# Performance work log

Hardware: AMD Instinct MI355X
Metric: run time of the kernel (lower is better)

## Reference

```python
import jax, jax.numpy as jnp
import numpy as np


def log_g(x):
    # log of g(x) where g(x) = x + 0.5 for x >= 0 else sigmoid(x)
    return jnp.where(x >= 0, jnp.log(jnp.where(x >= 0, x, 0.0) + 0.5), -jax.nn.softplus(-x))


def mingru_layer(x, h0, W, b):
    # x: (B,S,Din), h0: (B,1,H) positive, W: (2H,Din), b: (2H,)
    gh = jnp.einsum('bsd,ed->bse', x, W) + b
    gate, hidden = jnp.split(gh, 2, axis=-1)
    log_z = -jax.nn.softplus(-gate)        # log sigmoid(gate)
    log_coeffs = -jax.nn.softplus(gate)    # log (1 - sigmoid(gate))
    log_values = jnp.concatenate([jnp.log(h0), log_z + log_g(hidden)], axis=1)  # (B,S+1,H)
    a_star = jnp.pad(jnp.cumsum(log_coeffs, axis=1), ((0, 0), (1, 0), (0, 0)))  # (B,S+1,H)
    log_h = a_star + jax.lax.cumlogsumexp(log_values - a_star, axis=1)
    return jnp.exp(log_h)[:, 1:]  # (B,S,H)


def setup_inputs() -> dict:
    key = jax.random.key(0)
    ks = jax.random.split(key, 6)
    B, S, D, H = 8, 2048, 1024, 1024
    L = 2
    s = 0.02
    return {
        'x': jax.random.normal(ks[0], (B, S, D), jnp.float32),
        'h': jax.random.uniform(ks[1], (L, B, 1, H), jnp.float32, 0.05, 1.0),
        'w0': jax.random.normal(ks[2], (2 * H, D), jnp.float32) * s,
        'b0': jax.random.normal(ks[3], (2 * H,), jnp.float32) * s,
        'w1': jax.random.normal(ks[4], (2 * H, H), jnp.float32) * s,
        'b1': jax.random.normal(ks[5], (2 * H,), jnp.float32) * s,
    }


def reference(x, h, w0, b0, w1, b1):
    # layer 0 (residual, align = Identity since input_dims == hidden_dims)
    out0 = mingru_layer(x, h[0], w0, b0)
    h0_final = out0[:, -1:]
    inp = out0 + x
    # layer 1 (last layer: residual, no dropout after)
    out1 = mingru_layer(inp, h[1], w1, b1)
    h1_final = out1[:, -1:]
    out = out1 + inp
    h_final = jnp.stack([h0_final, h1_final])  # (L,B,1,H)
    return out, h_final
```

## Files before the change

### kernel.cpp

```cpp
#include <hip/hip_runtime.h>
#include <hip/hip_bf16.h>
#include <cstdint>
#include <cstddef>

#define GAS __attribute__((address_space(1)))
#define LAS __attribute__((address_space(3)))

typedef __attribute__((ext_vector_type(8))) __bf16 bf16x8;
typedef __attribute__((ext_vector_type(4))) float f32x4;

constexpr int kB = 8, kS = 2048, kK = 1024, kH = 1024;
constexpr int kM = kB * kS;
constexpr int kN2 = 2 * kH;
constexpr int BM = 256, BK = 32;
constexpr int NKT = kK / BK;

constexpr size_t kOffXb   = 0;
constexpr size_t kOffW0   = 33554432;
constexpr size_t kOffW1   = 37748736;
constexpr size_t kOffA    = 41943040;
constexpr size_t kOffG    = 75497472;
constexpr size_t kOffCA   = 109051904;
constexpr size_t kOffCV   = 111149056;
constexpr size_t kOffHst  = 113246208;
constexpr size_t kWsNeed  = 115343360;

__device__ __forceinline__ ushort f2bf(float f) {
    union { float f; uint32_t u; } v; v.f = f;
    uint32_t r = v.u + 0x7FFFu + ((v.u >> 16) & 1u);
    return (ushort)(r >> 16);
}
__device__ __forceinline__ float bf2f(ushort u) {
    union { uint32_t u; float f; } v; v.u = (uint32_t)u << 16;
    return v.f;
}

constexpr int QX = kM * kK / 4;
constexpr int QW = kN2 * kK / 4;
__global__ void cvt3_kernel(const float* __restrict__ x, const float* __restrict__ w0,
                            const float* __restrict__ w1,
                            ushort* __restrict__ xb, ushort* __restrict__ w0b,
                            ushort* __restrict__ w1b)
{
    int i = blockIdx.x * 256 + threadIdx.x;
    const float* s; ushort* d;
    if (i < QX)            { s = x  + (size_t)i * 4;            d = xb  + (size_t)i * 4; }
    else if (i < QX + QW)  { int k = i - QX;      s = w0 + (size_t)k * 4; d = w0b + (size_t)k * 4; }
    else                   { int k = i - QX - QW; s = w1 + (size_t)k * 4; d = w1b + (size_t)k * 4; }
    f32x4 v = *reinterpret_cast<const f32x4*>(s);
    ushort4 o;
    o.x = f2bf(v.x); o.y = f2bf(v.y); o.z = f2bf(v.z); o.w = f2bf(v.w);
    *reinterpret_cast<ushort4*>(d) = o;
}

__global__ __launch_bounds__(512, 1)
void gemm_scan_kernel(const ushort* __restrict__ A, const ushort* __restrict__ W,
                      const float* __restrict__ bias,
                      ushort* __restrict__ Apref, ushort* __restrict__ Vpref,
                      float* __restrict__ cA, float* __restrict__ cV)
{
    __shared__ ushort smem[69632];

    const int tid  = threadIdx.x;
    const int lane = tid & 63;
    const int wv   = tid >> 6;
    const int wm   = wv >> 2;
    const int wn   = wv & 3;

    const int bid = blockIdx.x;
    const int sid = (bid & 7) * 64 + (bid >> 3);
    const int tm  = sid >> 3;
    const int tn  = sid & 7;
    const int m0  = tm * BM;
    const int j0  = tn * 128;

    f32x4 acc[8][4];
#pragma unroll
    for (int i = 0; i < 8; ++i)
#pragma unroll
        for (int j = 0; j < 4; ++j) acc[i][j] = (f32x4){0.f, 0.f, 0.f, 0.f};

    const int srow  = wv * 16 + (lane >> 2);
    const int sslot = (lane & 3) ^ ((lane >> 3) & 3);
    const int scol  = sslot * 8;

    const ushort* ga0 = A + (size_t)(m0 + srow) * kK + scol;
    const ushort* ga1 = ga0 + (size_t)128 * kK;
    const ushort* gb0 = W + (size_t)(j0 + srow) * kK + scol;
    const ushort* gb1 = W + (size_t)(1024 + j0 + srow) * kK + scol;

    char* lds = (char*)smem;
    const int ldsw = wv * 1024;

    const int rslot = (lane >> 4) ^ ((lane >> 1) & 3);
    const int rb    = (lane & 15) * 64 + rslot * 16;
    const int aoff  = wm * 8192 + rb;
    const int boff  = 16384 + wn * 4096 + rb;

#define VMWAIT(N) asm volatile("s_waitcnt vmcnt(" #N ")" ::: "memory")

#define STAGE_A(SBUF) do {                                                       \
    __builtin_amdgcn_global_load_lds((const GAS void*)(ga0),                     \
        (LAS void*)(lds + (SBUF) * 32768 + ldsw),          16, 0, 0);            \
    __builtin_amdgcn_global_load_lds((const GAS void*)(ga1),                     \
        (LAS void*)(lds + (SBUF) * 32768 + 8192  + ldsw),  16, 0, 0);            \
  } while (0)

#define STAGE_B(SBUF) do {                                                       \
    __builtin_amdgcn_global_load_lds((const GAS void*)(gb0),                     \
        (LAS void*)(lds + (SBUF) * 32768 + 16384 + ldsw),  16, 0, 0);            \
    __builtin_amdgcn_global_load_lds((const GAS void*)(gb1),                     \
        (LAS void*)(lds + (SBUF) * 32768 + 24576 + ldsw),  16, 0, 0);            \
    ga0 += BK; ga1 += BK; gb0 += BK; gb1 += BK;                                  \
  } while (0)

#define TILE_GEN(BUF, SA, SB, EW) do {                                           \
    bf16x8 bf_[4], af_[4];                                                       \
    _Pragma("unroll")                                                            \
    for (int nf_ = 0; nf_ < 4; ++nf_)                                            \
        bf_[nf_] = *reinterpret_cast<const bf16x8*>(                             \
            lds + (BUF) * 32768 + boff + nf_ * 1024);                            \
    _Pragma("unroll")                                                            \
    for (int mf_ = 0; mf_ < 4; ++mf_)                                            \
        af_[mf_] = *reinterpret_cast<const bf16x8*>(                             \
            lds + (BUF) * 32768 + aoff + mf_ * 1024);                            \
    SA;                                                                          \
    __builtin_amdgcn_s_barrier();                                                \
    asm volatile("s_waitcnt lgkmcnt(0)" ::: "memory");                           \
    __builtin_amdgcn_sched_barrier(0);                                           \
    __builtin_amdgcn_s_setprio(1);                                               \
    _Pragma("unroll")                                                            \
    for (int mf_ = 0; mf_ < 4; ++mf_)                                            \
        _Pragma("unroll")                                                        \
        for (int nf_ = 0; nf_ < 4; ++nf_)                                        \
            acc[mf_][nf_] = __builtin_amdgcn_mfma_f32_16x16x32_bf16(             \
                af_[mf_], bf_[nf_], acc[mf_][nf_], 0, 0, 0);                     \
    __builtin_amdgcn_s_setprio(0);                                               \
    __builtin_amdgcn_s_barrier();                                                \
    _Pragma("unroll")                                                            \
    for (int mf_ = 0; mf_ < 4; ++mf_)                                            \
        af_[mf_] = *reinterpret_cast<const bf16x8*>(                             \
            lds + (BUF) * 32768 + aoff + 4096 + mf_ * 1024);                     \
    SB;                                                                          \
    __builtin_amdgcn_s_barrier();                                                \
    asm volatile("s_waitcnt lgkmcnt(0)" ::: "memory");                           \
    __builtin_amdgcn_sched_barrier(0);                                           \
    __builtin_amdgcn_s_setprio(1);                                               \
    _Pragma("unroll")                                                            \
    for (int mf_ = 0; mf_ < 4; ++mf_)                                            \
        _Pragma("unroll")                                                        \
        for (int nf_ = 0; nf_ < 4; ++nf_)                                        \
            acc[4 + mf_][nf_] = __builtin_amdgcn_mfma_f32_16x16x32_bf16(         \
                af_[mf_], bf_[nf_], acc[4 + mf_][nf_], 0, 0, 0);                 \
    __builtin_amdgcn_s_setprio(0);                                               \
    EW;                                                                          \
    __builtin_amdgcn_s_barrier();                                                \
  } while (0)

#define TILE(BUF, SBUF) TILE_GEN(BUF, STAGE_A(SBUF), STAGE_B(SBUF), VMWAIT(4))
#define TAIL0(BUF)      TILE_GEN(BUF, (void)0, (void)0, VMWAIT(0))
#define TAIL1(BUF)      TILE_GEN(BUF, (void)0, (void)0, (void)0)

    STAGE_A(0); STAGE_B(0);
    STAGE_A(1); STAGE_B(1);
    VMWAIT(4);
    __builtin_amdgcn_s_barrier();

    for (int g = 0; g < 7; ++g) {
        TILE(0, 2);
        TILE(1, 3);
        TILE(2, 0);
        TILE(3, 1);
    }
    TILE(0, 2);
    TILE(1, 3);
    TAIL0(2);
    TAIL1(3);

#undef TILE
#undef TAIL0
#undef TAIL1
#undef TILE_GEN
#undef STAGE_A
#undef STAGE_B
#undef VMWAIT

    ushort* a_lds = smem;
    ushort* g_lds = smem + 33792;
    float*  sumA  = (float*)(smem + 67584);
    float*  sumV  = sumA + 512;

    {
        const bool isG = (wn < 2);
        ushort* tgt = isG ? a_lds : g_lds;
        const int jl = (wn & 1) * 64;
        float bn[4];
#pragma unroll
        for (int nf = 0; nf < 4; ++nf)
            bn[nf] = bias[(isG ? 0 : 1024) + j0 + jl + nf * 16 + (lane & 15)];
#pragma unroll
        for (int mf = 0; mf < 8; ++mf) {
#pragma unroll
            for (int i = 0; i < 4; ++i) {
                const int m = wm * 128 + mf * 16 + (lane >> 4) * 4 + i;
#pragma unroll
                for (int nf = 0; nf < 4; ++nf) {
                    float val = acc[mf][nf][i] + bn[nf];
                    float r;
                    if (isG) r = 1.f / (1.f + __expf(val));
                    else     r = (val >= 0.f) ? val + 0.5f : 1.f / (1.f + __expf(-val));
                    tgt[m * 132 + jl + nf * 16 + (lane & 15)] = f2bf(r);
                }
            }
        }
    }
    __syncthreads();

    {
        const int j  = tid & 127;
        const int sg = tid >> 7;
        float A1 = 1.f, V1 = 0.f;
#pragma unroll 4
        for (int t = 0; t < 64; ++t) {
            const int s = sg * 64 + t;
            float a = bf2f(a_lds[s * 132 + j]);
            float g = bf2f(g_lds[s * 132 + j]);
            V1 = a * V1 + (1.f - a) * g;
            A1 *= a;
        }
        sumA[sg * 128 + j] = A1;
        sumV[sg * 128 + j] = V1;
        __syncthreads();
        float Ar = 1.f, Vr = 0.f;
        for (int k = 0; k < sg; ++k) {
            float Ak = sumA[k * 128 + j], Vk = sumV[k * 128 + j];
            Vr = Ak * Vr + Vk;
            Ar *= Ak;
        }
        ushort* ApG = Apref + (size_t)(m0 + sg * 64) * kH + j0 + j;
        ushort* VpG = Vpref + (size_t)(m0 + sg * 64) * kH + j0 + j;
#pragma unroll 4
        for (int t = 0; t < 64; ++t) {
            const int s = sg * 64 + t;
            float a = bf2f(a_lds[s * 132 + j]);
            float g = bf2f(g_lds[s * 132 + j]);
            Vr = a * Vr + (1.f - a) * g;
            Ar *= a;
            *ApG = f2bf(Ar);
            *VpG = f2bf(Vr);
            ApG += kH; VpG += kH;
        }
        if (sg == 3) {
            const int b = tm >> 3, c = tm & 7;
            cA[((b * 8 + c) << 10) + j0 + j] = Ar;
            cV[((b * 8 + c) << 10) + j0 + j] = Vr;
        }
    }
}

__global__ void scan_chunks_kernel(const float* __restrict__ cA, const float* __restrict__ cV,
                                   const float* __restrict__ h0, float* __restrict__ hstart,
                                   float* __restrict__ hfin)
{
    int idx = blockIdx.x * 256 + threadIdx.x;
    int j = idx & 1023, b = idx >> 10;
    float h = h0[(b << 10) + j];
    for (int c = 0; c < 8; ++c) {
        int o = ((b * 8 + c) << 10) + j;
        hstart[o] = h;
        h = cA[o] * h + cV[o];
    }
    hfin[(b << 10) + j] = h;
}

template<bool WRITE_F32>
__global__ void apply_kernel(const ushort* __restrict__ Ap, const ushort* __restrict__ Vp,
                             const float* __restrict__ hst, const ushort* __restrict__ res,
                             void* __restrict__ outp)
{
    size_t i = ((size_t)blockIdx.x * 256 + threadIdx.x) * 4;
    int m = (int)(i >> 10);
    int j = (int)(i & 1023);
    int b = m >> 11, s = m & 2047, c = s >> 8;
    f32x4 hcs = *reinterpret_cast<const f32x4*>(hst + (((b * 8 + c) << 10) + j));
    ushort4 Au = *reinterpret_cast<const ushort4*>(Ap + i);
    ushort4 Vu = *reinterpret_cast<const ushort4*>(Vp + i);
    ushort4 Ru = *reinterpret_cast<const ushort4*>(res + i);
    f32x4 o;
    o.x = bf2f(Au.x) * hcs.x + bf2f(Vu.x) + bf2f(Ru.x);
    o.y = bf2f(Au.y) * hcs.y + bf2f(Vu.y) + bf2f(Ru.y);
    o.z = bf2f(Au.z) * hcs.z + bf2f(Vu.z) + bf2f(Ru.z);
    o.w = bf2f(Au.w) * hcs.w + bf2f(Vu.w) + bf2f(Ru.w);
    if (WRITE_F32) {
        *reinterpret_cast<f32x4*>((float*)outp + i) = o;
    } else {
        ushort4 ob;
        ob.x = f2bf(o.x); ob.y = f2bf(o.y); ob.z = f2bf(o.z); ob.w = f2bf(o.w);
        *reinterpret_cast<ushort4*>((ushort*)outp + i) = ob;
    }
}

extern "C" void kernel_launch(void* const* d_in, const int* in_sizes, int n_in,
                              void* d_out, int out_size, void* d_ws, size_t ws_size,
                              hipStream_t stream)
{
    const float* x  = (const float*)d_in[0];
    const float* h  = (const float*)d_in[1];
    const float* w0 = (const float*)d_in[2];
    const float* b0 = (const float*)d_in[3];
    const float* w1 = (const float*)d_in[4];
    const float* b1 = (const float*)d_in[5];
    float* out = (float*)d_out;
    char* ws = (char*)d_ws;

    if (ws_size < kWsNeed) return;

    ushort* xb   = (ushort*)(ws + kOffXb);
    ushort* inpb = (ushort*)(ws + kOffXb);
    ushort* w0b  = (ushort*)(ws + kOffW0);
    ushort* w1b  = (ushort*)(ws + kOffW1);
    ushort* Ap   = (ushort*)(ws + kOffA);
    ushort* Vp   = (ushort*)(ws + kOffG);
    float*  cA   = (float*)(ws + kOffCA);
    float*  cV   = (float*)(ws + kOffCV);
    float*  hst  = (float*)(ws + kOffHst);

    float* out_h = out + (size_t)kM * kH;

    cvt3_kernel<<<(QX + 2 * QW) / 256, 256, 0, stream>>>(x, w0, w1, xb, w0b, w1b);

    const int gemm_grid  = (kM / BM) * (kN2 / 256);
    const int apply_grid = kM * kH / 4 / 256;

    gemm_scan_kernel<<<gemm_grid, 512, 0, stream>>>(xb, w0b, b0, Ap, Vp, cA, cV);
    scan_chunks_kernel<<<32, 256, 0, stream>>>(cA, cV, h, hst, out_h);
    apply_kernel<false><<<apply_grid, 256, 0, stream>>>(Ap, Vp, hst, xb, inpb);

    gemm_scan_kernel<<<gemm_grid, 512, 0, stream>>>(inpb, w1b, b1, Ap, Vp, cA, cV);
    scan_chunks_kernel<<<32, 256, 0, stream>>>(cA, cV, h + (size_t)kB * kH, hst, out_h + (size_t)kB * kH);
    apply_kernel<true><<<apply_grid, 256, 0, stream>>>(Ap, Vp, hst, inpb, out);
}
```

Measured before the change: 270.9 us.

## Restructure GEMM main loop to BK=64 with two-stage double buffering

The K-step doubles from 32 to 64. The four-stage 32KB LDS ring becomes a two-stage 64KB ring, and each tile is split into four phases that each issue part of the next tile's global-to-LDS loads. Loop iterations and loop overhead are halved. The prefetch distance is shorter, and the vmcnt waits now sit mid-tile, so global-load latency may be less well hidden.

```diff
diff --git a/kernel.cpp b/kernel.cpp
--- a/kernel.cpp
+++ b/kernel.cpp
@@ -12,7 +12,7 @@
 constexpr int kB = 8, kS = 2048, kK = 1024, kH = 1024;
 constexpr int kM = kB * kS;
 constexpr int kN2 = 2 * kH;
-constexpr int BM = 256, BK = 32;
+constexpr int BM = 256, BK = 64;
 constexpr int NKT = kK / BK;
 
 constexpr size_t kOffXb   = 0;
@@ -95,94 +95,116 @@
     const int rslot = (lane >> 4) ^ ((lane >> 1) & 3);
     const int rb    = (lane & 15) * 64 + rslot * 16;
     const int aoff  = wm * 8192 + rb;
-    const int boff  = 16384 + wn * 4096 + rb;
+    const int boff  = 32768 + wn * 4096 + rb;
 
 #define VMWAIT(N) asm volatile("s_waitcnt vmcnt(" #N ")" ::: "memory")
 
-#define STAGE_A(SBUF) do {                                                       \
-    __builtin_amdgcn_global_load_lds((const GAS void*)(ga0),                     \
-        (LAS void*)(lds + (SBUF) * 32768 + ldsw),          16, 0, 0);            \
-    __builtin_amdgcn_global_load_lds((const GAS void*)(ga1),                     \
-        (LAS void*)(lds + (SBUF) * 32768 + 8192  + ldsw),  16, 0, 0);            \
+#define STG_A(SBUF, KH) do {                                                     \
+    __builtin_amdgcn_global_load_lds((const GAS void*)(ga0 + (KH) * 32),         \
+        (LAS void*)(lds + (SBUF) * 65536 + (KH) * 16384 + ldsw),        16, 0, 0); \
+    __builtin_amdgcn_global_load_lds((const GAS void*)(ga1 + (KH) * 32),         \
+        (LAS void*)(lds + (SBUF) * 65536 + (KH) * 16384 + 8192 + ldsw), 16, 0, 0); \
   } while (0)
 
-#define STAGE_B(SBUF) do {                                                       \
-    __builtin_amdgcn_global_load_lds((const GAS void*)(gb0),                     \
-        (LAS void*)(lds + (SBUF) * 32768 + 16384 + ldsw),  16, 0, 0);            \
-    __builtin_amdgcn_global_load_lds((const GAS void*)(gb1),                     \
-        (LAS void*)(lds + (SBUF) * 32768 + 24576 + ldsw),  16, 0, 0);            \
-    ga0 += BK; ga1 += BK; gb0 += BK; gb1 += BK;                                  \
+#define STG_B(SBUF, KH) do {                                                     \
+    __builtin_amdgcn_global_load_lds((const GAS void*)(gb0 + (KH) * 32),         \
+        (LAS void*)(lds + (SBUF) * 65536 + 32768 + (KH) * 16384 + ldsw), 16, 0, 0); \
+    __builtin_amdgcn_global_load_lds((const GAS void*)(gb1 + (KH) * 32),         \
+        (LAS void*)(lds + (SBUF) * 65536 + 32768 + (KH) * 16384 + 8192 + ldsw), 16, 0, 0); \
   } while (0)
 
-#define TILE_GEN(BUF, SA, SB, EW) do {                                           \
+#define PH_SYNC                                                                  \
+    __builtin_amdgcn_s_barrier();                                                \
+    asm volatile("s_waitcnt lgkmcnt(0)" ::: "memory");                           \
+    __builtin_amdgcn_sched_barrier(0)
+
+#define MFMA16(BASE)                                                             \
+    __builtin_amdgcn_s_setprio(1);                                               \
+    _Pragma("unroll")                                                            \
+    for (int mf_ = 0; mf_ < 4; ++mf_)                                            \
+        _Pragma("unroll")                                                        \
+        for (int nf_ = 0; nf_ < 4; ++nf_)                                        \
+            acc[(BASE) + mf_][nf_] = __builtin_amdgcn_mfma_f32_16x16x32_bf16(    \
+                af_[mf_], bf_[nf_], acc[(BASE) + mf_][nf_], 0, 0, 0);            \
+    __builtin_amdgcn_s_setprio(0)
+
+#define TILE64(BUF, S0, S1, S2, S3, EW1, EW3) do {                               \
     bf16x8 bf_[4], af_[4];                                                       \
+                          \
     _Pragma("unroll")                                                            \
     for (int nf_ = 0; nf_ < 4; ++nf_)                                            \
         bf_[nf_] = *reinterpret_cast<const bf16x8*>(                             \
-            lds + (BUF) * 32768 + boff + nf_ * 1024);                            \
+            lds + (BUF) * 65536 + boff + nf_ * 1024);                            \
     _Pragma("unroll")                                                            \
     for (int mf_ = 0; mf_ < 4; ++mf_)                                            \
         af_[mf_] = *reinterpret_cast<const bf16x8*>(                             \
-            lds + (BUF) * 32768 + aoff + mf_ * 1024);                            \
-    SA;                                                                          \
-    __builtin_amdgcn_s_barrier();                                                \
-    asm volatile("s_waitcnt lgkmcnt(0)" ::: "memory");                           \
-    __builtin_amdgcn_sched_barrier(0);                                           \
-    __builtin_amdgcn_s_setprio(1);                                               \
-    _Pragma("unroll")                                                            \
-    for (int mf_ = 0; mf_ < 4; ++mf_)                                            \
-        _Pragma("unroll")                                                        \
-        for (int nf_ = 0; nf_ < 4; ++nf_)                                        \
-            acc[mf_][nf_] = __builtin_amdgcn_mfma_f32_16x16x32_bf16(             \
-                af_[mf_], bf_[nf_], acc[mf_][nf_], 0, 0, 0);                     \
-    __builtin_amdgcn_s_setprio(0);                                               \
-    __builtin_amdgcn_s_barrier();                                                \
+            lds + (BUF) * 65536 + aoff + mf_ * 1024);                            \
+    S0;                                                                          \
+    PH_SYNC;                                                                     \
+    MFMA16(0);                                                                   \
+    __builtin_amdgcn_s_barrier();                                                \
+                                                \
     _Pragma("unroll")                                                            \
     for (int mf_ = 0; mf_ < 4; ++mf_)                                            \
         af_[mf_] = *reinterpret_cast<const bf16x8*>(                             \
-            lds + (BUF) * 32768 + aoff + 4096 + mf_ * 1024);                     \
-    SB;                                                                          \
-    __builtin_amdgcn_s_barrier();                                                \
-    asm volatile("s_waitcnt lgkmcnt(0)" ::: "memory");                           \
-    __builtin_amdgcn_sched_barrier(0);                                           \
-    __builtin_amdgcn_s_setprio(1);                                               \
-    _Pragma("unroll")                                                            \
-    for (int mf_ = 0; mf_ < 4; ++mf_)                                            \
-        _Pragma("unroll")                                                        \
-        for (int nf_ = 0; nf_ < 4; ++nf_)                                        \
-            acc[4 + mf_][nf_] = __builtin_amdgcn_mfma_f32_16x16x32_bf16(         \
-                af_[mf_], bf_[nf_], acc[4 + mf_][nf_], 0, 0, 0);                 \
-    __builtin_amdgcn_s_setprio(0);                                               \
-    EW;                                                                          \
+            lds + (BUF) * 65536 + aoff + 4096 + mf_ * 1024);                     \
+    S1;                                                                          \
+    PH_SYNC;                                                                     \
+    MFMA16(4);                                                                   \
+    EW1;                                                                         \
+    __builtin_amdgcn_s_barrier();                                                \
+                                                             \
+    _Pragma("unroll")                                                            \
+    for (int nf_ = 0; nf_ < 4; ++nf_)                                            \
+        bf_[nf_] = *reinterpret_cast<const bf16x8*>(                             \
+            lds + (BUF) * 65536 + 16384 + boff + nf_ * 1024);                    \
+    _Pragma("unroll")                                                            \
+    for (int mf_ = 0; mf_ < 4; ++mf_)                                            \
+        af_[mf_] = *reinterpret_cast<const bf16x8*>(                             \
+            lds + (BUF) * 65536 + 16384 + aoff + mf_ * 1024);                    \
+    S2;                                                                          \
+    PH_SYNC;                                                                     \
+    MFMA16(0);                                                                   \
+    __builtin_amdgcn_s_barrier();                                                \
+                                                             \
+    _Pragma("unroll")                                                            \
+    for (int mf_ = 0; mf_ < 4; ++mf_)                                            \
+        af_[mf_] = *reinterpret_cast<const bf16x8*>(                             \
+            lds + (BUF) * 65536 + 16384 + aoff + 4096 + mf_ * 1024);             \
+    S3;                                                                          \
+    PH_SYNC;                                                                     \
+    MFMA16(4);                                                                   \
+    EW3;                                                                         \
     __builtin_amdgcn_s_barrier();                                                \
   } while (0)
 
-#define TILE(BUF, SBUF) TILE_GEN(BUF, STAGE_A(SBUF), STAGE_B(SBUF), VMWAIT(4))
-#define TAIL0(BUF)      TILE_GEN(BUF, (void)0, (void)0, VMWAIT(0))
-#define TAIL1(BUF)      TILE_GEN(BUF, (void)0, (void)0, (void)0)
-
-    STAGE_A(0); STAGE_B(0);
-    STAGE_A(1); STAGE_B(1);
+#define ADV do { ga0 += BK; ga1 += BK; gb0 += BK; gb1 += BK; } while (0)
+#define TILE(BUF) TILE64(BUF,                                                    \
+    STG_A((BUF) ^ 1, 0), STG_B((BUF) ^ 1, 0),                                    \
+    STG_A((BUF) ^ 1, 1), do { STG_B((BUF) ^ 1, 1); ADV; } while (0),             \
+    VMWAIT(4), VMWAIT(4))
+#define TAIL(BUF) TILE64(BUF, (void)0, (void)0, (void)0, (void)0, VMWAIT(0), (void)0)
+
+    STG_A(0, 0); STG_B(0, 0); STG_A(0, 1); STG_B(0, 1);
+    ADV;
     VMWAIT(4);
     __builtin_amdgcn_s_barrier();
 
     for (int g = 0; g < 7; ++g) {
-        TILE(0, 2);
-        TILE(1, 3);
-        TILE(2, 0);
-        TILE(3, 1);
-    }
-    TILE(0, 2);
-    TILE(1, 3);
-    TAIL0(2);
-    TAIL1(3);
+        TILE(0);
+        TILE(1);
+    }
+    TILE(0);
+    TAIL(1);
 
 #undef TILE
-#undef TAIL0
-#undef TAIL1
-#undef TILE_GEN
-#undef STAGE_A
-#undef STAGE_B
+#undef TAIL
+#undef TILE64
+#undef MFMA16
+#undef PH_SYNC
+#undef STG_A
+#undef STG_B
+#undef ADV
 #undef VMWAIT
 
     ushort* a_lds = smem;
```

Result: no change. 270.3 us (-0.2%).

## Halve GEMM row tile to 128 with 2 blocks per CU and vectorized chunk scan

Applied to the files above, without the earlier changes.

Reworks the fused GEMM+scan kernel to use 128-row tiles with 256 threads and two resident blocks per CU. The LDS pipeline changes from four stages to three, and the sequence is split into 16 chunks instead of 8. The in-block scan now processes four hidden columns per thread with vector LDS loads and global stores. The aim is better occupancy and latency hiding, plus fewer serial scan steps per thread. The cost is that each block loads W for fewer rows, so more global traffic per FLOP, and the cross-chunk scan gets longer.

```diff
diff --git a/kernel.cpp b/kernel.cpp
--- a/kernel.cpp
+++ b/kernel.cpp
@@ -12,8 +12,9 @@
 constexpr int kB = 8, kS = 2048, kK = 1024, kH = 1024;
 constexpr int kM = kB * kS;
 constexpr int kN2 = 2 * kH;
-constexpr int BM = 256, BK = 32;
+constexpr int BM = 128, BK = 32;
 constexpr int NKT = kK / BK;
+constexpr int kChunks = 16;
 
 constexpr size_t kOffXb   = 0;
 constexpr size_t kOffW0   = 33554432;
@@ -21,8 +22,8 @@
 constexpr size_t kOffA    = 41943040;
 constexpr size_t kOffG    = 75497472;
 constexpr size_t kOffCA   = 109051904;
-constexpr size_t kOffCV   = 111149056;
-constexpr size_t kOffHst  = 113246208;
+constexpr size_t kOffCV   = 109576192;
+constexpr size_t kOffHst  = 110100480;
 constexpr size_t kWsNeed  = 115343360;
 
 __device__ __forceinline__ ushort f2bf(float f) {
@@ -53,77 +54,82 @@
     *reinterpret_cast<ushort4*>(d) = o;
 }
 
-__global__ __launch_bounds__(512, 1)
+__global__ __launch_bounds__(256, 2)
 void gemm_scan_kernel(const ushort* __restrict__ A, const ushort* __restrict__ W,
                       const float* __restrict__ bias,
                       ushort* __restrict__ Apref, ushort* __restrict__ Vpref,
                       float* __restrict__ cA, float* __restrict__ cV)
 {
-    __shared__ ushort smem[69632];
+    __shared__ ushort smem[37888];
 
     const int tid  = threadIdx.x;
     const int lane = tid & 63;
     const int wv   = tid >> 6;
-    const int wm   = wv >> 2;
-    const int wn   = wv & 3;
+    const int wm   = wv >> 1;
+    const int wn   = wv & 1;
 
     const int bid = blockIdx.x;
-    const int sid = (bid & 7) * 64 + (bid >> 3);
+    const int sid = (bid & 7) * 128 + (bid >> 3);
     const int tm  = sid >> 3;
     const int tn  = sid & 7;
     const int m0  = tm * BM;
     const int j0  = tn * 128;
-
-    f32x4 acc[8][4];
-#pragma unroll
-    for (int i = 0; i < 8; ++i)
-#pragma unroll
-        for (int j = 0; j < 4; ++j) acc[i][j] = (f32x4){0.f, 0.f, 0.f, 0.f};
-
-    const int srow  = wv * 16 + (lane >> 2);
-    const int sslot = (lane & 3) ^ ((lane >> 3) & 3);
+    const int b   = tm >> 4;
+    const int c   = tm & 15;
+
+    f32x4 acc[4][8];
+#pragma unroll
+    for (int i = 0; i < 4; ++i)
+#pragma unroll
+        for (int j = 0; j < 8; ++j) acc[i][j] = (f32x4){0.f, 0.f, 0.f, 0.f};
+
+    const int srow  = tid >> 2;
+    const int sslot = (tid & 3) ^ ((tid >> 3) & 3);
     const int scol  = sslot * 8;
+    const int tid16 = tid * 16;
 
     const ushort* ga0 = A + (size_t)(m0 + srow) * kK + scol;
-    const ushort* ga1 = ga0 + (size_t)128 * kK;
     const ushort* gb0 = W + (size_t)(j0 + srow) * kK + scol;
     const ushort* gb1 = W + (size_t)(1024 + j0 + srow) * kK + scol;
 
     char* lds = (char*)smem;
-    const int ldsw = wv * 1024;
 
     const int rslot = (lane >> 4) ^ ((lane >> 1) & 3);
     const int rb    = (lane & 15) * 64 + rslot * 16;
-    const int aoff  = wm * 8192 + rb;
-    const int boff  = 16384 + wn * 4096 + rb;
+    const int aoff  = wm * 4096 + rb;
+    const int boff  = 8192 + wn * 8192 + rb;
 
 #define VMWAIT(N) asm volatile("s_waitcnt vmcnt(" #N ")" ::: "memory")
 
-#define STAGE_A(SBUF) do {                                                       \
+#define STG3A(S) do {                                                            \
     __builtin_amdgcn_global_load_lds((const GAS void*)(ga0),                     \
-        (LAS void*)(lds + (SBUF) * 32768 + ldsw),          16, 0, 0);            \
-    __builtin_amdgcn_global_load_lds((const GAS void*)(ga1),                     \
-        (LAS void*)(lds + (SBUF) * 32768 + 8192  + ldsw),  16, 0, 0);            \
+        (LAS void*)(lds + (S) * 24576 + tid16),          16, 0, 0);              \
+    __builtin_amdgcn_global_load_lds((const GAS void*)(ga0 + 65536),             \
+        (LAS void*)(lds + (S) * 24576 + 4096 + tid16),   16, 0, 0);              \
+    __builtin_amdgcn_global_load_lds((const GAS void*)(gb0),                     \
+        (LAS void*)(lds + (S) * 24576 + 8192 + tid16),   16, 0, 0);              \
   } while (0)
 
-#define STAGE_B(SBUF) do {                                                       \
-    __builtin_amdgcn_global_load_lds((const GAS void*)(gb0),                     \
-        (LAS void*)(lds + (SBUF) * 32768 + 16384 + ldsw),  16, 0, 0);            \
+#define STG3B(S) do {                                                            \
+    __builtin_amdgcn_global_load_lds((const GAS void*)(gb0 + 65536),             \
+        (LAS void*)(lds + (S) * 24576 + 12288 + tid16),  16, 0, 0);              \
     __builtin_amdgcn_global_load_lds((const GAS void*)(gb1),                     \
-        (LAS void*)(lds + (SBUF) * 32768 + 24576 + ldsw),  16, 0, 0);            \
-    ga0 += BK; ga1 += BK; gb0 += BK; gb1 += BK;                                  \
+        (LAS void*)(lds + (S) * 24576 + 16384 + tid16),  16, 0, 0);              \
+    __builtin_amdgcn_global_load_lds((const GAS void*)(gb1 + 65536),             \
+        (LAS void*)(lds + (S) * 24576 + 20480 + tid16),  16, 0, 0);              \
+    ga0 += BK; gb0 += BK; gb1 += BK;                                             \
   } while (0)
 
 #define TILE_GEN(BUF, SA, SB, EW) do {                                           \
-    bf16x8 bf_[4], af_[4];                                                       \
+    bf16x8 af_[4], bf_[4];                                                       \
+    _Pragma("unroll")                                                            \
+    for (int mf_ = 0; mf_ < 4; ++mf_)                                            \
+        af_[mf_] = *reinterpret_cast<const bf16x8*>(                             \
+            lds + (BUF) * 24576 + aoff + mf_ * 1024);                            \
     _Pragma("unroll")                                                            \
     for (int nf_ = 0; nf_ < 4; ++nf_)                                            \
         bf_[nf_] = *reinterpret_cast<const bf16x8*>(                             \
-            lds + (BUF) * 32768 + boff + nf_ * 1024);                            \
-    _Pragma("unroll")                                                            \
-    for (int mf_ = 0; mf_ < 4; ++mf_)                                            \
-        af_[mf_] = *reinterpret_cast<const bf16x8*>(                             \
-            lds + (BUF) * 32768 + aoff + mf_ * 1024);                            \
+            lds + (BUF) * 24576 + boff + nf_ * 1024);                            \
     SA;                                                                          \
     __builtin_amdgcn_s_barrier();                                                \
     asm volatile("s_waitcnt lgkmcnt(0)" ::: "memory");                           \
@@ -138,9 +144,9 @@
     __builtin_amdgcn_s_setprio(0);                                               \
     __builtin_amdgcn_s_barrier();                                                \
     _Pragma("unroll")                                                            \
-    for (int mf_ = 0; mf_ < 4; ++mf_)                                            \
-        af_[mf_] = *reinterpret_cast<const bf16x8*>(                             \
-            lds + (BUF) * 32768 + aoff + 4096 + mf_ * 1024);                     \
+    for (int nf_ = 0; nf_ < 4; ++nf_)                                            \
+        bf_[nf_] = *reinterpret_cast<const bf16x8*>(                             \
+            lds + (BUF) * 24576 + boff + (4 + nf_) * 1024);                      \
     SB;                                                                          \
     __builtin_amdgcn_s_barrier();                                                \
     asm volatile("s_waitcnt lgkmcnt(0)" ::: "memory");                           \
@@ -150,66 +156,62 @@
     for (int mf_ = 0; mf_ < 4; ++mf_)                                            \
         _Pragma("unroll")                                                        \
         for (int nf_ = 0; nf_ < 4; ++nf_)                                        \
-            acc[4 + mf_][nf_] = __builtin_amdgcn_mfma_f32_16x16x32_bf16(         \
-                af_[mf_], bf_[nf_], acc[4 + mf_][nf_], 0, 0, 0);                 \
+            acc[mf_][4 + nf_] = __builtin_amdgcn_mfma_f32_16x16x32_bf16(         \
+                af_[mf_], bf_[nf_], acc[mf_][4 + nf_], 0, 0, 0);                 \
     __builtin_amdgcn_s_setprio(0);                                               \
     EW;                                                                          \
     __builtin_amdgcn_s_barrier();                                                \
   } while (0)
 
-#define TILE(BUF, SBUF) TILE_GEN(BUF, STAGE_A(SBUF), STAGE_B(SBUF), VMWAIT(4))
+#define TILE(BUF, SBUF) TILE_GEN(BUF, STG3A(SBUF), STG3B(SBUF), VMWAIT(6))
 #define TAIL0(BUF)      TILE_GEN(BUF, (void)0, (void)0, VMWAIT(0))
 #define TAIL1(BUF)      TILE_GEN(BUF, (void)0, (void)0, (void)0)
 
-    STAGE_A(0); STAGE_B(0);
-    STAGE_A(1); STAGE_B(1);
-    VMWAIT(4);
+    STG3A(0); STG3B(0);
+    STG3A(1); STG3B(1);
+    VMWAIT(6);
     __builtin_amdgcn_s_barrier();
 
-    for (int g = 0; g < 7; ++g) {
+    for (int g = 0; g < 10; ++g) {
         TILE(0, 2);
-        TILE(1, 3);
-        TILE(2, 0);
-        TILE(3, 1);
-    }
-    TILE(0, 2);
-    TILE(1, 3);
-    TAIL0(2);
-    TAIL1(3);
+        TILE(1, 0);
+        TILE(2, 1);
+    }
+    TAIL0(0);
+    TAIL1(1);
 
 #undef TILE
 #undef TAIL0
 #undef TAIL1
 #undef TILE_GEN
-#undef STAGE_A
-#undef STAGE_B
+#undef STG3A
+#undef STG3B
 #undef VMWAIT
 
     ushort* a_lds = smem;
-    ushort* g_lds = smem + 33792;
-    float*  sumA  = (float*)(smem + 67584);
-    float*  sumV  = sumA + 512;
+    ushort* g_lds = smem + 16896;
+    f32x4*  sA4   = (f32x4*)(lds + 67584);
+    f32x4*  sV4   = (f32x4*)(lds + 71680);
 
     {
-        const bool isG = (wn < 2);
+        const bool isG = (wn == 0);
         ushort* tgt = isG ? a_lds : g_lds;
-        const int jl = (wn & 1) * 64;
-        float bn[4];
-#pragma unroll
-        for (int nf = 0; nf < 4; ++nf)
-            bn[nf] = bias[(isG ? 0 : 1024) + j0 + jl + nf * 16 + (lane & 15)];
-#pragma unroll
-        for (int mf = 0; mf < 8; ++mf) {
+        float bn[8];
+#pragma unroll
+        for (int nf = 0; nf < 8; ++nf)
+            bn[nf] = bias[(isG ? 0 : 1024) + j0 + nf * 16 + (lane & 15)];
+#pragma unroll
+        for (int mf = 0; mf < 4; ++mf) {
 #pragma unroll
             for (int i = 0; i < 4; ++i) {
-                const int m = wm * 128 + mf * 16 + (lane >> 4) * 4 + i;
-#pragma unroll
-                for (int nf = 0; nf < 4; ++nf) {
+                const int m = wm * 64 + mf * 16 + (lane >> 4) * 4 + i;
+#pragma unroll
+                for (int nf = 0; nf < 8; ++nf) {
                     float val = acc[mf][nf][i] + bn[nf];
                     float r;
                     if (isG) r = 1.f / (1.f + __expf(val));
                     else     r = (val >= 0.f) ? val + 0.5f : 1.f / (1.f + __expf(-val));
-                    tgt[m * 132 + jl + nf * 16 + (lane & 15)] = f2bf(r);
+                    tgt[m * 132 + nf * 16 + (lane & 15)] = f2bf(r);
                 }
             }
         }
@@ -217,43 +219,52 @@
     __syncthreads();
 
     {
-        const int j  = tid & 127;
-        const int sg = tid >> 7;
-        float A1 = 1.f, V1 = 0.f;
+        const int jq = tid & 31;
+        const int sg = tid >> 5;
+        f32x4 A1 = (f32x4){1.f, 1.f, 1.f, 1.f};
+        f32x4 V1 = (f32x4){0.f, 0.f, 0.f, 0.f};
 #pragma unroll 4
-        for (int t = 0; t < 64; ++t) {
-            const int s = sg * 64 + t;
-            float a = bf2f(a_lds[s * 132 + j]);
-            float g = bf2f(g_lds[s * 132 + j]);
+        for (int t = 0; t < 16; ++t) {
+            const int s = sg * 16 + t;
+            ushort4 au = *reinterpret_cast<const ushort4*>(a_lds + s * 132 + jq * 4);
+            ushort4 gu = *reinterpret_cast<const ushort4*>(g_lds + s * 132 + jq * 4);
+            f32x4 a = (f32x4){bf2f(au.x), bf2f(au.y), bf2f(au.z), bf2f(au.w)};
+            f32x4 g = (f32x4){bf2f(gu.x), bf2f(gu.y), bf2f(gu.z), bf2f(gu.w)};
             V1 = a * V1 + (1.f - a) * g;
             A1 *= a;
         }
-        sumA[sg * 128 + j] = A1;
-        sumV[sg * 128 + j] = V1;
+        sA4[sg * 32 + jq] = A1;
+        sV4[sg * 32 + jq] = V1;
         __syncthreads();
-        float Ar = 1.f, Vr = 0.f;
+        f32x4 Ar = (f32x4){1.f, 1.f, 1.f, 1.f};
+        f32x4 Vr = (f32x4){0.f, 0.f, 0.f, 0.f};
         for (int k = 0; k < sg; ++k) {
-            float Ak = sumA[k * 128 + j], Vk = sumV[k * 128 + j];
+            f32x4 Ak = sA4[k * 32 + jq], Vk = sV4[k * 32 + jq];
             Vr = Ak * Vr + Vk;
             Ar *= Ak;
         }
-        ushort* ApG = Apref + (size_t)(m0 + sg * 64) * kH + j0 + j;
-        ushort* VpG = Vpref + (size_t)(m0 + sg * 64) * kH + j0 + j;
+        ushort* ApG = Apref + (size_t)(m0 + sg * 16) * kH + j0 + jq * 4;
+        ushort* VpG = Vpref + (size_t)(m0 + sg * 16) * kH + j0 + jq * 4;
 #pragma unroll 4
-        for (int t = 0; t < 64; ++t) {
-            const int s = sg * 64 + t;
-            float a = bf2f(a_lds[s * 132 + j]);
-            float g = bf2f(g_lds[s * 132 + j]);
+        for (int t = 0; t < 16; ++t) {
+            const int s = sg * 16 + t;
+            ushort4 au = *reinterpret_cast<const ushort4*>(a_lds + s * 132 + jq * 4);
+            ushort4 gu = *reinterpret_cast<const ushort4*>(g_lds + s * 132 + jq * 4);
+            f32x4 a = (f32x4){bf2f(au.x), bf2f(au.y), bf2f(au.z), bf2f(au.w)};
+            f32x4 g = (f32x4){bf2f(gu.x), bf2f(gu.y), bf2f(gu.z), bf2f(gu.w)};
             Vr = a * Vr + (1.f - a) * g;
             Ar *= a;
-            *ApG = f2bf(Ar);
-            *VpG = f2bf(Vr);
+            ushort4 oa, ov;
+            oa.x = f2bf(Ar.x); oa.y = f2bf(Ar.y); oa.z = f2bf(Ar.z); oa.w = f2bf(Ar.w);
+            ov.x = f2bf(Vr.x); ov.y = f2bf(Vr.y); ov.z = f2bf(Vr.z); ov.w = f2bf(Vr.w);
+            *reinterpret_cast<ushort4*>(ApG) = oa;
+            *reinterpret_cast<ushort4*>(VpG) = ov;
             ApG += kH; VpG += kH;
         }
-        if (sg == 3) {
-            const int b = tm >> 3, c = tm & 7;
-            cA[((b * 8 + c) << 10) + j0 + j] = Ar;
-            cV[((b * 8 + c) << 10) + j0 + j] = Vr;
+        if (sg == 7) {
+            size_t o = ((size_t)(b * kChunks + c) << 10) + j0 + jq * 4;
+            *reinterpret_cast<f32x4*>(cA + o) = Ar;
+            *reinterpret_cast<f32x4*>(cV + o) = Vr;
         }
     }
 }
@@ -263,14 +274,14 @@
                                    float* __restrict__ hfin)
 {
     int idx = blockIdx.x * 256 + threadIdx.x;
-    int j = idx & 1023, b = idx >> 10;
-    float h = h0[(b << 10) + j];
-    for (int c = 0; c < 8; ++c) {
-        int o = ((b * 8 + c) << 10) + j;
+    int j = idx & 1023, bb = idx >> 10;
+    float h = h0[(bb << 10) + j];
+    for (int c = 0; c < kChunks; ++c) {
+        int o = ((bb * kChunks + c) << 10) + j;
         hstart[o] = h;
         h = cA[o] * h + cV[o];
     }
-    hfin[(b << 10) + j] = h;
+    hfin[(bb << 10) + j] = h;
 }
 
 template<bool WRITE_F32>
@@ -281,8 +292,8 @@
     size_t i = ((size_t)blockIdx.x * 256 + threadIdx.x) * 4;
     int m = (int)(i >> 10);
     int j = (int)(i & 1023);
-    int b = m >> 11, s = m & 2047, c = s >> 8;
-    f32x4 hcs = *reinterpret_cast<const f32x4*>(hst + (((b * 8 + c) << 10) + j));
+    int bb = m >> 11, s = m & 2047, c = s >> 7;
+    f32x4 hcs = *reinterpret_cast<const f32x4*>(hst + (((bb * kChunks + c) << 10) + j));
     ushort4 Au = *reinterpret_cast<const ushort4*>(Ap + i);
     ushort4 Vu = *reinterpret_cast<const ushort4*>(Vp + i);
     ushort4 Ru = *reinterpret_cast<const ushort4*>(res + i);
@@ -332,11 +343,11 @@
     const int gemm_grid  = (kM / BM) * (kN2 / 256);
     const int apply_grid = kM * kH / 4 / 256;
 
-    gemm_scan_kernel<<<gemm_grid, 512, 0, stream>>>(xb, w0b, b0, Ap, Vp, cA, cV);
+    gemm_scan_kernel<<<gemm_grid, 256, 0, stream>>>(xb, w0b, b0, Ap, Vp, cA, cV);
     scan_chunks_kernel<<<32, 256, 0, stream>>>(cA, cV, h, hst, out_h);
     apply_kernel<false><<<apply_grid, 256, 0, stream>>>(Ap, Vp, hst, xb, inpb);
 
-    gemm_scan_kernel<<<gemm_grid, 512, 0, stream>>>(inpb, w1b, b1, Ap, Vp, cA, cV);
+    gemm_scan_kernel<<<gemm_grid, 256, 0, stream>>>(inpb, w1b, b1, Ap, Vp, cA, cV);
     scan_chunks_kernel<<<32, 256, 0, stream>>>(cA, cV, h + (size_t)kB * kH, hst, out_h + (size_t)kB * kH);
     apply_kernel<true><<<apply_grid, 256, 0, stream>>>(Ap, Vp, hst, inpb, out);
 }
```

Result: no change. 269.1 us, median of 2 (-0.7%).
